# Optimization experiments

Measured on AMD Instinct MI355X. Metric: run time of the kernel, lower is better.

The kernel has to match this reference:

```python
import jax, jax.numpy as jnp
import numpy as np

H, HD, CHUNK = 16, 64, 128


def _rotary(x):
    # x: (B,H,N,d); rotary_embedding_torch default: interleaved pairs, theta=10000
    N, d = x.shape[-2], x.shape[-1]
    inv_freq = 1.0 / (10000.0 ** (jnp.arange(0, d, 2, dtype=jnp.float32) / d))
    ang = jnp.arange(N, dtype=jnp.float32)[:, None] * inv_freq[None, :]  # (N, d/2)
    ang = jnp.repeat(ang, 2, axis=-1)  # (N, d), each freq repeated twice
    cos, sin = jnp.cos(ang), jnp.sin(ang)
    x1, x2 = x[..., 0::2], x[..., 1::2]
    xr = jnp.stack([-x2, x1], axis=-1).reshape(x.shape)  # rotate_half (interleaved)
    return x * cos + xr * sin


def _split_heads(t, B, N):
    return t.reshape(B, N, H, HD).transpose(0, 2, 1, 3)  # (B,H,N,Hd)


def _chunked(Q, KK, VK):
    # chunk-parallel linear-attention recurrence: per-token outer products,
    # intra-chunk cumsum, carried state across chunks, Frobenius normalization.
    B, h, N, d = Q.shape
    nc = N // CHUNK

    def to_chunks(t):
        return t.reshape(B, h, nc, CHUNK, d).transpose(2, 0, 1, 3, 4)  # (nc,B,h,c,d)

    S0 = jnp.eye(d, dtype=Q.dtype) * jnp.sqrt(jnp.float32(d))
    S0 = jnp.broadcast_to(S0, (B, h, d, d))

    def step(SK_state, inp):
        q, kk, vk = inp  # (B,h,c,d)
        ok = jnp.einsum('bhni,bhnj->bhnij', kk, vk)            # outer products
        SK = jnp.cumsum(ok, axis=2) + SK_state[:, :, None]      # prefix-sum + carry
        norm = jnp.sqrt(jnp.sum(SK * SK, axis=(-2, -1), keepdims=True)) + 1e-8
        SKn = SK / norm                                         # Frobenius-normalized
        y = jnp.einsum('bhni,bhnji->bhnj', q, SKn)              # q @ SK^T per token
        return SK[:, :, -1], y

    _, ys = jax.lax.scan(step, S0, (to_chunks(Q), to_chunks(KK), to_chunks(VK)))
    return ys.transpose(1, 2, 0, 3, 4).reshape(B, h, N, d)


def setup_inputs():
    key = jax.random.key(0)
    ks = jax.random.split(key, 5)
    B, N, D = 2, 2048, 1024
    X = jax.random.normal(ks[0], (B, N, D), jnp.float32)
    w_qkv = jax.random.normal(ks[1], (D, 3 * H * HD), jnp.float32) * 0.02
    w_kvkv = jax.random.normal(ks[2], (D, 4 * H * HD), jnp.float32) * 0.02
    w_out = jax.random.normal(ks[3], (H * HD, D), jnp.float32) * 0.02
    b_out = jnp.zeros((D,), jnp.float32)
    return {"X": X, "w_qkv": w_qkv, "w_kvkv": w_kvkv, "w_out": w_out, "b_out": b_out}


def reference(X, w_qkv, w_kvkv, w_out, b_out):
    B, N, D = X.shape
    q, k, v = jnp.split(X @ w_qkv, 3, axis=-1)
    Q = _split_heads(q, B, N)
    K = _split_heads(k, B, N)
    V = _split_heads(v, B, N)
    kk, vk, _kv, _vv = jnp.split(X @ w_kvkv, 4, axis=-1)
    KK = _split_heads(kk, B, N)
    VK = _split_heads(vk, B, N)
    # NOTE: the SV branch (KV, VV) in the original is returned by the chunked fn
    # but never used by forward's output, so it is dead code for the fwd result.
    Qn = _chunked(Q, KK, VK)
    Qr = _rotary(Qn)
    Kr = _rotary(K)
    scale = 1.0 / jnp.sqrt(jnp.float32(HD))
    scores = jnp.einsum('bhqd,bhkd->bhqk', Qr, Kr) * scale
    mask = jnp.tril(jnp.ones((N, N), dtype=bool))
    scores = jnp.where(mask, scores, -jnp.inf)
    attn = jax.nn.softmax(scores, axis=-1)
    out = jnp.einsum('bhqk,bhkd->bhqd', attn, V)
    out = out.transpose(0, 2, 1, 3).reshape(B, N, H * HD)
    return out @ w_out + b_out
```

## Files before the change

### kernel.cpp

```cpp
#include <hip/hip_runtime.h>

typedef unsigned int u32;
typedef unsigned short u16;
typedef __attribute__((ext_vector_type(8))) __bf16 bf16x8;
typedef __attribute__((ext_vector_type(4))) float f32x4;

constexpr int NH = 16;
constexpr int HDM = 64;
constexpr int NSQ = 2048;
constexpr int KD = 1024;
constexpr int BHT = 32;
constexpr float ROT_C = 13.287712379549449f / 32.0f;

__device__ __forceinline__ u16 f2bf(float f) {
  u32 u = __float_as_uint(f);
  u += 0x7fffu + ((u >> 16) & 1u);
  return (u16)(u >> 16);
}
__device__ __forceinline__ float bf2f(u16 h) {
  return __uint_as_float(((u32)h) << 16);
}

__device__ __forceinline__ void fast_sincos(float th, float* s, float* c) {
  __sincosf(th, s, c);
}

__device__ __forceinline__ void gl_lds16(const u16* g, u16* l) {
  __builtin_amdgcn_global_load_lds(
      (const __attribute__((address_space(1))) u32*)g,
      (__attribute__((address_space(3))) u32*)l, 16, 0, 0);
}

__device__ __forceinline__ bf16x8 ldf(const u16* b, int row, int cb, int rs) {
  return *(const bf16x8*)((const char*)b + row * rs + ((cb * 16) ^ ((row & 7) << 4)));
}

__global__ void k_f32_to_bf16(const float* __restrict__ src, u16* __restrict__ dst, int n4) {
  int i = blockIdx.x * 256 + threadIdx.x;
  if (i < n4) {
    float4 v = ((const float4*)src)[i];
    ushort4 o;
    o.x = f2bf(v.x); o.y = f2bf(v.y); o.z = f2bf(v.z); o.w = f2bf(v.w);
    ((ushort4*)dst)[i] = o;
  }
}

__global__ void k_transpose_bf16(const float* __restrict__ src, int srcld,
                                 u16* __restrict__ dst, int dstld) {
  __shared__ float tile[64][65];
  int ct = blockIdx.x * 64, kt = blockIdx.y * 64;
  int lc = threadIdx.x & 63, rg = threadIdx.x >> 6;
#pragma unroll
  for (int i = 0; i < 16; ++i) {
    int kl = rg * 16 + i;
    tile[kl][lc] = src[(size_t)(kt + kl) * srcld + ct + lc];
  }
  __syncthreads();
#pragma unroll
  for (int i = 0; i < 16; ++i) {
    int cl = rg * 16 + i;
    dst[(size_t)(ct + cl) * dstld + kt + lc] = f2bf(tile[lc][cl]);
  }
}

__device__ __forceinline__ void stage256(const u16* __restrict__ gA, const u16* __restrict__ gB,
                                         u16* AL, u16* BL, int mt, int nt, int kt, int tid) {
#pragma unroll
  for (int l = 0; l < 4; ++l) {
    int off = l * 8192 + tid * 16;
    int row = off >> 7;
    int cb = (off >> 4) & 7;
    int col = (cb ^ (row & 7)) << 3;
    gl_lds16(gA + (size_t)(mt * 256 + row) * KD + kt * 64 + col, AL + (off >> 1));
  }
#pragma unroll
  for (int l = 0; l < 4; ++l) {
    int off = l * 8192 + tid * 16;
    int row = off >> 7;
    int cb = (off >> 4) & 7;
    int col = (cb ^ (row & 7)) << 3;
    gl_lds16(gB + (size_t)(nt * 256 + row) * KD + kt * 64 + col, BL + (off >> 1));
  }
}

__device__ __forceinline__ void compute256(const u16* AL, const u16* BL,
                                           f32x4 (&acc)[8][4], int wr, int wc, int g, int q) {
#pragma unroll
  for (int ks = 0; ks < 2; ++ks) {
    bf16x8 bfr[4];
#pragma unroll
    for (int nf = 0; nf < 4; ++nf)
      bfr[nf] = ldf(BL, wc * 64 + nf * 16 + q, ks * 4 + g, 128);
#pragma unroll
    for (int mh = 0; mh < 2; ++mh) {
      bf16x8 af[4];
#pragma unroll
      for (int mf = 0; mf < 4; ++mf)
        af[mf] = ldf(AL, wr * 128 + (mh * 4 + mf) * 16 + q, ks * 4 + g, 128);
      __builtin_amdgcn_s_setprio(1);
#pragma unroll
      for (int mf = 0; mf < 4; ++mf)
#pragma unroll
        for (int nf = 0; nf < 4; ++nf)
          acc[mh * 4 + mf][nf] =
              __builtin_amdgcn_mfma_f32_16x16x32_bf16(af[mf], bfr[nf], acc[mh * 4 + mf][nf], 0, 0, 0);
      __builtin_amdgcn_s_setprio(0);
    }
  }
}

__global__ __launch_bounds__(512) void k_gemm0_256(const u16* __restrict__ A,
                                                   const u16* __restrict__ Bt,
                                                   u16* __restrict__ o0, u16* __restrict__ o1,
                                                   u16* __restrict__ o2, u16* __restrict__ o3,
                                                   u16* __restrict__ o4) {
  __shared__ __align__(16) u16 AL[2][16384];
  __shared__ __align__(16) u16 BL[2][16384];
  int bid = blockIdx.x;
  int swz = (bid & 7) * 40 + (bid >> 3);
  int nt = swz % 20, mt = swz / 20;
  int tid = threadIdx.x, w = tid >> 6, lane = tid & 63;
  int g = lane >> 4, q = lane & 15;
  int wr = w >> 2, wc = w & 3;

  f32x4 acc[8][4];
#pragma unroll
  for (int m = 0; m < 8; ++m)
#pragma unroll
    for (int n = 0; n < 4; ++n) acc[m][n] = (f32x4){0.f, 0.f, 0.f, 0.f};

  stage256(A, Bt, AL[0], BL[0], mt, nt, 0, tid);
  stage256(A, Bt, AL[1], BL[1], mt, nt, 1, tid);
  asm volatile("s_waitcnt vmcnt(8)" ::: "memory");
  __builtin_amdgcn_s_barrier();
  __builtin_amdgcn_sched_barrier(0);

#define GBODY(KT, PBUF)                                                     \
  {                                                                         \
    compute256(AL[PBUF], BL[PBUF], acc, wr, wc, g, q);                      \
    __builtin_amdgcn_s_barrier();                                           \
    if ((KT) + 2 < 16) {                                                    \
      stage256(A, Bt, AL[PBUF], BL[PBUF], mt, nt, (KT) + 2, tid);           \
      asm volatile("s_waitcnt vmcnt(8)" ::: "memory");                      \
    } else if ((KT) == 14) {                                                \
      asm volatile("s_waitcnt vmcnt(0)" ::: "memory");                      \
    }                                                                       \
    __builtin_amdgcn_s_barrier();                                           \
    __builtin_amdgcn_sched_barrier(0);                                      \
  }

  for (int it = 0; it < 8; ++it) {
    GBODY(2 * it, 0);
    GBODY(2 * it + 1, 1);
  }
#undef GBODY

#pragma unroll
  for (int nf = 0; nf < 4; ++nf) {
    int c = nt * 256 + wc * 64 + nf * 16 + q;
    int t = c >> 10;
    if (t == 1) {
      int rem = c & 1023;
      int hh = rem >> 6, dd = rem & 63;
      float invf = exp2f(-(float)(dd >> 1) * ROT_C);
      float sgn = (dd & 1) ? 1.0f : -1.0f;
      size_t hoff = (size_t)hh * NSQ * HDM + dd;
#pragma unroll
      for (int mf = 0; mf < 8; ++mf)
#pragma unroll
        for (int r = 0; r < 4; ++r) {
          int row = mt * 256 + wr * 128 + mf * 16 + g * 4 + r;
          int b = row >> 11, nn = row & 2047;
          float mine = acc[mf][nf][r];
          float part = __shfl_xor(mine, 1);
          float s, cc;
          fast_sincos((float)nn * invf, &s, &cc);
          o1[(size_t)b * NH * NSQ * HDM + hoff + (size_t)nn * HDM] = f2bf(mine * cc + sgn * part * s);
        }
    } else if (t == 2) {
      int rem = c & 1023;
      int hh = rem >> 6, dd = rem & 63;
#pragma unroll
      for (int mf = 0; mf < 8; ++mf)
#pragma unroll
        for (int r = 0; r < 4; ++r) {
          int row = mt * 256 + wr * 128 + mf * 16 + g * 4 + r;
          int b = row >> 11, nn = row & 2047;
          o2[((size_t)(b * NH + hh) * HDM + dd) * NSQ + nn] = f2bf(acc[mf][nf][r]);
        }
    } else {
      u16* dst = (t == 0) ? o0 : ((t == 3) ? o3 : o4);
      int rem = c & 1023;
      size_t hoff = (size_t)(rem >> 6) * NSQ * HDM + (rem & 63);
#pragma unroll
      for (int mf = 0; mf < 8; ++mf)
#pragma unroll
        for (int r = 0; r < 4; ++r) {
          int row = mt * 256 + wr * 128 + mf * 16 + g * 4 + r;
          int b = row >> 11, nn = row & 2047;
          dst[(size_t)b * NH * NSQ * HDM + hoff + (size_t)nn * HDM] = f2bf(acc[mf][nf][r]);
        }
    }
  }
}

__device__ __forceinline__ void gemm_stage1(const u16* __restrict__ A, const u16* __restrict__ Bt,
                                            u16* Albuf, u16* Blbuf, int mt, int nt, int kt,
                                            int w, int lane) {
#pragma unroll
  for (int i = 0; i < 2; ++i) {
    int ob = (w * 2 + i) * 1024 + lane * 16;
    int row = ob >> 6;
    int ke = (ob & 63) >> 1;
    int grow = mt * 128 + row;
    int k = kt * 32 + ke;
    const u16* ga = A + ((size_t)((grow >> 11) * NH + (k >> 6)) * NSQ + (grow & 2047)) * HDM + (k & 63);
    gl_lds16(ga, Albuf + (w * 2 + i) * 512);
    const u16* gb = Bt + (size_t)(nt * 128 + row) * KD + kt * 32 + ke;
    gl_lds16(gb, Blbuf + (w * 2 + i) * 512);
  }
}

__device__ __forceinline__ void gemm_compute1(const u16* Albuf, const u16* Blbuf,
                                              f32x4 acc[4][4], int wr, int wc, int g, int q) {
  bf16x8 af[4], bfr[4];
#pragma unroll
  for (int m = 0; m < 4; ++m)
    af[m] = *(const bf16x8*)(Albuf + (wr * 64 + m * 16 + q) * 32 + g * 8);
#pragma unroll
  for (int n = 0; n < 4; ++n)
    bfr[n] = *(const bf16x8*)(Blbuf + (wc * 64 + n * 16 + q) * 32 + g * 8);
#pragma unroll
  for (int m = 0; m < 4; ++m)
#pragma unroll
    for (int n = 0; n < 4; ++n)
      acc[m][n] = __builtin_amdgcn_mfma_f32_16x16x32_bf16(af[m], bfr[n], acc[m][n], 0, 0, 0);
}

__global__ __launch_bounds__(256) void k_gemm_out(const u16* __restrict__ A, const u16* __restrict__ Bt,
                                                  const float* __restrict__ bias,
                                                  float* __restrict__ Cout) {
  __shared__ __align__(16) u16 Al[2][4096];
  __shared__ __align__(16) u16 Bl[2][4096];
  int nt = blockIdx.x, mt = blockIdx.y;
  int tid = threadIdx.x, w = tid >> 6, lane = tid & 63;
  int g = lane >> 4, q = lane & 15, wr = w >> 1, wc = w & 1;
  f32x4 acc[4][4];
#pragma unroll
  for (int m = 0; m < 4; ++m)
#pragma unroll
    for (int n = 0; n < 4; ++n) acc[m][n] = (f32x4){0.f, 0.f, 0.f, 0.f};

  gemm_stage1(A, Bt, Al[0], Bl[0], mt, nt, 0, w, lane);
  __syncthreads();
  int cur = 0;
  for (int kt = 1; kt < 32; ++kt) {
    gemm_stage1(A, Bt, Al[cur ^ 1], Bl[cur ^ 1], mt, nt, kt, w, lane);
    gemm_compute1(Al[cur], Bl[cur], acc, wr, wc, g, q);
    __syncthreads();
    cur ^= 1;
  }
  gemm_compute1(Al[cur], Bl[cur], acc, wr, wc, g, q);

#pragma unroll
  for (int nf = 0; nf < 4; ++nf) {
    int c = nt * 128 + wc * 64 + nf * 16 + q;
    float bv = bias[c];
#pragma unroll
    for (int mf = 0; mf < 4; ++mf)
#pragma unroll
      for (int r = 0; r < 4; ++r) {
        int row = mt * 128 + wr * 64 + mf * 16 + g * 4 + r;
        Cout[(size_t)row * 1024 + c] = acc[mf][nf][r] + bv;
      }
  }
}

__global__ __launch_bounds__(256) void k_chunk_outer(const u16* __restrict__ Kk,
                                                     const u16* __restrict__ Vk,
                                                     float* __restrict__ Mc) {
  int bhc = blockIdx.x;
  __shared__ float kk[128][64];
  __shared__ float vv[128][64];
  int tid = threadIdx.x;
  size_t base = ((size_t)(bhc >> 4) * NSQ + (size_t)(bhc & 15) * 128) * HDM;
  for (int i = tid; i < 2048; i += 256) {
    int r = i >> 4, c4 = (i & 15) * 4;
    ushort4 a = ((const ushort4*)(Kk + base))[i];
    kk[r][c4] = bf2f(a.x); kk[r][c4 + 1] = bf2f(a.y); kk[r][c4 + 2] = bf2f(a.z); kk[r][c4 + 3] = bf2f(a.w);
    ushort4 b = ((const ushort4*)(Vk + base))[i];
    vv[r][c4] = bf2f(b.x); vv[r][c4 + 1] = bf2f(b.y); vv[r][c4 + 2] = bf2f(b.z); vv[r][c4 + 3] = bf2f(b.w);
  }
  __syncthreads();
  int i0 = (tid >> 4) * 4, j0 = (tid & 15) * 4;
  float a2[4][4];
#pragma unroll
  for (int di = 0; di < 4; ++di)
#pragma unroll
    for (int dj = 0; dj < 4; ++dj) a2[di][dj] = 0.f;
  for (int m = 0; m < 128; ++m) {
    float ka[4], vb[4];
#pragma unroll
    for (int d = 0; d < 4; ++d) { ka[d] = kk[m][i0 + d]; vb[d] = vv[m][j0 + d]; }
#pragma unroll
    for (int di = 0; di < 4; ++di)
#pragma unroll
      for (int dj = 0; dj < 4; ++dj) a2[di][dj] += ka[di] * vb[dj];
  }
  float* out = Mc + (size_t)bhc * 4096;
#pragma unroll
  for (int di = 0; di < 4; ++di) {
    float4 v = make_float4(a2[di][0], a2[di][1], a2[di][2], a2[di][3]);
    *(float4*)(out + (i0 + di) * 64 + j0) = v;
  }
}

__global__ __launch_bounds__(256) void k_chunk_prefix2(const float* __restrict__ Mc,
                                                       float* __restrict__ Sst) {
  int bh = blockIdx.x, rg = blockIdx.y;
  int tid = threadIdx.x;
  int r8 = tid >> 5, cp = tid & 31;
  int i = rg * 8 + r8, j0 = cp * 2;
  float s0 = (i == j0) ? 8.0f : 0.0f;
  float s1 = (i == j0 + 1) ? 8.0f : 0.0f;
  size_t rowoff = (size_t)i * 64 + j0;
  for (int c = 0; c < 16; ++c) {
    size_t o = ((size_t)bh * 16 + c) * 4096 + rowoff;
    *(float2*)(Sst + o) = make_float2(s0, s1);
    float2 mv = *(const float2*)(Mc + o);
    s0 += mv.x; s1 += mv.y;
  }
}

__global__ __launch_bounds__(256) void k_chunk_norm(const u16* __restrict__ Kk,
                                                    const u16* __restrict__ Vk,
                                                    const float* __restrict__ Sst,
                                                    float* __restrict__ Invn) {
  __shared__ __align__(16) u16 KkL[128 * 64];
  __shared__ __align__(16) u16 VkL[128 * 64];
  __shared__ __align__(16) u16 SL[64 * 64];
  __shared__ float prebuf[128][2];
  __shared__ float bilbuf[128][2];
  __shared__ float sc[128];
  __shared__ float red[4];
  int bhc = blockIdx.x;
  int tid = threadIdx.x, w = tid >> 6, lane = tid & 63;
  int g = lane >> 4, q = lane & 15;
  size_t base = (size_t)bhc * 8192;

  for (int ic = tid; ic < 1024; ic += 256) {
    int row = ic >> 3, cb = ic & 7;
    int off = row * 128 + ((cb * 16) ^ ((row & 7) << 4));
    *(uint4*)((char*)KkL + off) = ((const uint4*)(Kk + base))[ic];
    *(uint4*)((char*)VkL + off) = ((const uint4*)(Vk + base))[ic];
  }
  float ss = 0.f;
  const float4* Sg = (const float4*)(Sst + (size_t)bhc * 4096);
  for (int i = tid; i < 1024; i += 256) {
    float4 v = Sg[i];
    ss += v.x * v.x + v.y * v.y + v.z * v.z + v.w * v.w;
    int row = i >> 4, c8 = (i & 15) * 8;
    u32 lo = (u32)f2bf(v.x) | ((u32)f2bf(v.y) << 16);
    u32 hi = (u32)f2bf(v.z) | ((u32)f2bf(v.w) << 16);
    *(uint2*)((char*)SL + row * 128 + (c8 ^ ((row & 7) << 4))) = make_uint2(lo, hi);
  }
#pragma unroll
  for (int d = 1; d < 64; d <<= 1) ss += __shfl_xor(ss, d);
  if (lane == 0) red[w] = ss;
  __syncthreads();

  int wr = w >> 1, wc = w & 1;
  bf16x8 ka[4][2], va[4][2];
#pragma unroll
  for (int mf = 0; mf < 4; ++mf)
#pragma unroll
    for (int ks = 0; ks < 2; ++ks) {
      ka[mf][ks] = ldf(KkL, wr * 64 + mf * 16 + q, ks * 4 + g, 128);
      va[mf][ks] = ldf(VkL, wr * 64 + mf * 16 + q, ks * 4 + g, 128);
    }

  float pracc[4][4];
#pragma unroll
  for (int mf = 0; mf < 4; ++mf)
#pragma unroll
    for (int r = 0; r < 4; ++r) pracc[mf][r] = 0.f;
  for (int pf = 0; pf < 4; ++pf) {
    bf16x8 kb0 = ldf(KkL, wc * 64 + pf * 16 + q, g, 128);
    bf16x8 kb1 = ldf(KkL, wc * 64 + pf * 16 + q, 4 + g, 128);
    bf16x8 vb0 = ldf(VkL, wc * 64 + pf * 16 + q, g, 128);
    bf16x8 vb1 = ldf(VkL, wc * 64 + pf * 16 + q, 4 + g, 128);
#pragma unroll
    for (int mf = 0; mf < 4; ++mf) {
      f32x4 a1 = (f32x4){0.f, 0.f, 0.f, 0.f}, b1 = (f32x4){0.f, 0.f, 0.f, 0.f};
      a1 = __builtin_amdgcn_mfma_f32_16x16x32_bf16(ka[mf][0], kb0, a1, 0, 0, 0);
      a1 = __builtin_amdgcn_mfma_f32_16x16x32_bf16(ka[mf][1], kb1, a1, 0, 0, 0);
      b1 = __builtin_amdgcn_mfma_f32_16x16x32_bf16(va[mf][0], vb0, b1, 0, 0, 0);
      b1 = __builtin_amdgcn_mfma_f32_16x16x32_bf16(va[mf][1], vb1, b1, 0, 0, 0);
#pragma unroll
      for (int r = 0; r < 4; ++r) {
        int m = wr * 64 + mf * 16 + g * 4 + r;
        int p = wc * 64 + pf * 16 + q;
        float gv = a1[r] * b1[r];
        float coef = (p < m) ? 1.f : ((p == m) ? 0.5f : 0.f);
        pracc[mf][r] += coef * gv;
      }
    }
  }
#pragma unroll
  for (int mf = 0; mf < 4; ++mf)
#pragma unroll
    for (int r = 0; r < 4; ++r) {
      float v = pracc[mf][r];
      v += __shfl_xor(v, 1); v += __shfl_xor(v, 2); v += __shfl_xor(v, 4); v += __shfl_xor(v, 8);
      pracc[mf][r] = v;
    }
  if (q == 0) {
#pragma unroll
    for (int mf = 0; mf < 4; ++mf)
#pragma unroll
      for (int r = 0; r < 4; ++r) prebuf[wr * 64 + mf * 16 + g * 4 + r][wc] = pracc[mf][r];
  }

  float bacc[4][4];
#pragma unroll
  for (int mf = 0; mf < 4; ++mf)
#pragma unroll
    for (int r = 0; r < 4; ++r) bacc[mf][r] = 0.f;
  for (int jf = 0; jf < 2; ++jf) {
    bf16x8 sb0 = ldf(SL, wc * 32 + jf * 16 + q, g, 128);
    bf16x8 sb1 = ldf(SL, wc * 32 + jf * 16 + q, 4 + g, 128);
#pragma unroll
    for (int mf = 0; mf < 4; ++mf) {
      f32x4 u = (f32x4){0.f, 0.f, 0.f, 0.f};
      u = __builtin_amdgcn_mfma_f32_16x16x32_bf16(va[mf][0], sb0, u, 0, 0, 0);
      u = __builtin_amdgcn_mfma_f32_16x16x32_bf16(va[mf][1], sb1, u, 0, 0, 0);
#pragma unroll
      for (int r = 0; r < 4; ++r) {
        int m = wr * 64 + mf * 16 + g * 4 + r;
        int j = wc * 32 + jf * 16 + q;
        float kkv = bf2f(*(const u16*)((const char*)KkL + m * 128 + ((j * 2) ^ ((m & 7) << 4))));
        bacc[mf][r] += u[r] * kkv;
      }
    }
  }
#pragma unroll
  for (int mf = 0; mf < 4; ++mf)
#pragma unroll
    for (int r = 0; r < 4; ++r) {
      float v = bacc[mf][r];
      v += __shfl_xor(v, 1); v += __shfl_xor(v, 2); v += __shfl_xor(v, 4); v += __shfl_xor(v, 8);
      bacc[mf][r] = v;
    }
  if (q == 0) {
#pragma unroll
    for (int mf = 0; mf < 4; ++mf)
#pragma unroll
      for (int r = 0; r < 4; ++r) bilbuf[wr * 64 + mf * 16 + g * 4 + r][wc] = bacc[mf][r];
  }
  __syncthreads();

  if (tid < 128)
    sc[tid] = 2.f * (prebuf[tid][0] + prebuf[tid][1] + bilbuf[tid][0] + bilbuf[tid][1]);
  __syncthreads();
  for (int off = 1; off < 128; off <<= 1) {
    float add = 0.f;
    if (tid < 128 && tid >= off) add = sc[tid - off];
    __syncthreads();
    if (tid < 128) sc[tid] += add;
    __syncthreads();
  }
  if (tid < 128) {
    float n0 = red[0] + red[1] + red[2] + red[3];
    float cum = n0 + sc[tid];
    Invn[(size_t)bhc * 128 + tid] = 1.f / (sqrtf(cum) + 1e-8f);
  }
}

__global__ __launch_bounds__(256) void k_chunk_yv2(const u16* __restrict__ Qb,
                                                   const u16* __restrict__ Kk,
                                                   const u16* __restrict__ Vk,
                                                   const float* __restrict__ Sst,
                                                   const float* __restrict__ Invn,
                                                   u16* __restrict__ Qro) {
  __shared__ __align__(16) u16 QL[128 * 64];
  __shared__ __align__(16) u16 WL[128 * 64];
  __shared__ __align__(16) u16 SL[64 * 64];
  __shared__ __align__(16) u16 PL[128 * 128];
  __shared__ float inv[128];
  int bhc = blockIdx.x;
  int tid = threadIdx.x, w = tid >> 6, lane = tid & 63;
  int g = lane >> 4, q = lane & 15;
  size_t base = (size_t)bhc * 8192;

  for (int ic = tid; ic < 1024; ic += 256) {
    int row = ic >> 3, cb = ic & 7;
    int off = row * 128 + ((cb * 16) ^ ((row & 7) << 4));
    *(uint4*)((char*)QL + off) = ((const uint4*)(Qb + base))[ic];
    *(uint4*)((char*)WL + off) = ((const uint4*)(Vk + base))[ic];
  }
  const float4* Sg = (const float4*)(Sst + (size_t)bhc * 4096);
  for (int i = tid; i < 1024; i += 256) {
    float4 v = Sg[i];
    int row = i >> 4, c8 = (i & 15) * 8;
    u32 lo = (u32)f2bf(v.x) | ((u32)f2bf(v.y) << 16);
    u32 hi = (u32)f2bf(v.z) | ((u32)f2bf(v.w) << 16);
    *(uint2*)((char*)SL + row * 128 + (c8 ^ ((row & 7) << 4))) = make_uint2(lo, hi);
  }
  if (tid < 128) inv[tid] = Invn[(size_t)bhc * 128 + tid];
  __syncthreads();

  int wr = w >> 1, wc = w & 1;
  f32x4 pacc[4][4];
#pragma unroll
  for (int mf = 0; mf < 4; ++mf)
#pragma unroll
    for (int nf = 0; nf < 4; ++nf) pacc[mf][nf] = (f32x4){0.f, 0.f, 0.f, 0.f};
#pragma unroll
  for (int ks = 0; ks < 2; ++ks) {
    bf16x8 av[4], bq[4];
#pragma unroll
    for (int mf = 0; mf < 4; ++mf) av[mf] = ldf(WL, wr * 64 + mf * 16 + q, ks * 4 + g, 128);
#pragma unroll
    for (int nf = 0; nf < 4; ++nf) bq[nf] = ldf(QL, wc * 64 + nf * 16 + q, ks * 4 + g, 128);
#pragma unroll
    for (int mf = 0; mf < 4; ++mf)
#pragma unroll
      for (int nf = 0; nf < 4; ++nf)
        pacc[mf][nf] = __builtin_amdgcn_mfma_f32_16x16x32_bf16(av[mf], bq[nf], pacc[mf][nf], 0, 0, 0);
  }
#pragma unroll
  for (int mf = 0; mf < 4; ++mf)
#pragma unroll
    for (int nf = 0; nf < 4; ++nf) {
      int m0 = wr * 64 + mf * 16 + g * 4;
      int n = wc * 64 + nf * 16 + q;
      float v0 = (m0 + 0 <= n) ? pacc[mf][nf][0] : 0.f;
      float v1 = (m0 + 1 <= n) ? pacc[mf][nf][1] : 0.f;
      float v2 = (m0 + 2 <= n) ? pacc[mf][nf][2] : 0.f;
      float v3 = (m0 + 3 <= n) ? pacc[mf][nf][3] : 0.f;
      u32 lo = (u32)f2bf(v0) | ((u32)f2bf(v1) << 16);
      u32 hi = (u32)f2bf(v2) | ((u32)f2bf(v3) << 16);
      *(uint2*)((char*)PL + n * 256 + ((m0 * 2) ^ ((n & 7) << 4))) = make_uint2(lo, hi);
    }
  __syncthreads();
  for (int i = tid; i < 2048; i += 256) {
    int r = i >> 4, c4 = (i & 15) * 4;
    ushort4 kv = ((const ushort4*)(Kk + base))[i];
    *(u16*)((char*)WL + (c4 + 0) * 256 + ((r * 2) ^ (((c4 + 0) & 7) << 4))) = kv.x;
    *(u16*)((char*)WL + (c4 + 1) * 256 + ((r * 2) ^ (((c4 + 1) & 7) << 4))) = kv.y;
    *(u16*)((char*)WL + (c4 + 2) * 256 + ((r * 2) ^ (((c4 + 2) & 7) << 4))) = kv.z;
    *(u16*)((char*)WL + (c4 + 3) * 256 + ((r * 2) ^ (((c4 + 3) & 7) << 4))) = kv.w;
  }
  __syncthreads();

  f32x4 yacc[4][2];
#pragma unroll
  for (int nf = 0; nf < 4; ++nf)
#pragma unroll
    for (int jf = 0; jf < 2; ++jf) yacc[nf][jf] = (f32x4){0.f, 0.f, 0.f, 0.f};
#pragma unroll
  for (int ks = 0; ks < 2; ++ks) {
    bf16x8 aq[4], bs[2];
#pragma unroll
    for (int nf = 0; nf < 4; ++nf) aq[nf] = ldf(QL, wr * 64 + nf * 16 + q, ks * 4 + g, 128);
#pragma unroll
    for (int jf = 0; jf < 2; ++jf) bs[jf] = ldf(SL, wc * 32 + jf * 16 + q, ks * 4 + g, 128);
#pragma unroll
    for (int nf = 0; nf < 4; ++nf)
#pragma unroll
      for (int jf = 0; jf < 2; ++jf)
        yacc[nf][jf] = __builtin_amdgcn_mfma_f32_16x16x32_bf16(aq[nf], bs[jf], yacc[nf][jf], 0, 0, 0);
  }
#pragma unroll
  for (int ks = 0; ks < 4; ++ks) {
    bf16x8 ap[4], bk[2];
#pragma unroll
    for (int nf = 0; nf < 4; ++nf) ap[nf] = ldf(PL, wr * 64 + nf * 16 + q, ks * 4 + g, 256);
#pragma unroll
    for (int jf = 0; jf < 2; ++jf) bk[jf] = ldf(WL, wc * 32 + jf * 16 + q, ks * 4 + g, 256);
#pragma unroll
    for (int nf = 0; nf < 4; ++nf)
#pragma unroll
      for (int jf = 0; jf < 2; ++jf)
        yacc[nf][jf] = __builtin_amdgcn_mfma_f32_16x16x32_bf16(ap[nf], bk[jf], yacc[nf][jf], 0, 0, 0);
  }
#pragma unroll
  for (int nf = 0; nf < 4; ++nf)
#pragma unroll
    for (int jf = 0; jf < 2; ++jf) {
      int j = wc * 32 + jf * 16 + q;
      float invf = exp2f(-(float)(j >> 1) * ROT_C);
      float sgn = (j & 1) ? 1.0f : -1.0f;
#pragma unroll
      for (int r = 0; r < 4; ++r) {
        int n = wr * 64 + nf * 16 + g * 4 + r;
        float val = yacc[nf][jf][r] * inv[n];
        float part = __shfl_xor(val, 1);
        int ng = (bhc & 15) * 128 + n;
        float s, cc;
        fast_sincos((float)ng * invf, &s, &cc);
        Qro[base + (size_t)n * 64 + j] = f2bf((val * cc + sgn * part * s) * 0.125f);
      }
    }
}

__global__ __launch_bounds__(512) void k_attn2(const u16* __restrict__ Qr, const u16* __restrict__ Kr,
                                               const u16* __restrict__ Vt, u16* __restrict__ Ob) {
  __shared__ __align__(16) u16 QL[128 * 64];
  __shared__ __align__(16) u16 KL[2][64 * 64];
  __shared__ __align__(16) u16 VL[2][64 * 64];
  __shared__ __align__(16) u16 PLa[8][16 * 64];
  int bh = blockIdx.x, pair = blockIdx.y;
  int tid = threadIdx.x, w = tid >> 6, lane = tid & 63;
  int g = lane >> 4, q16 = lane & 15;
  const u16* Qg_base = Qr + (size_t)bh * NSQ * HDM;
  const u16* Kg_base = Kr + (size_t)bh * NSQ * HDM;
  const u16* VTg_base = Vt + (size_t)bh * HDM * NSQ;
  u16* Og_base = Ob + (size_t)bh * NSQ * HDM;
  u16* Pw = PLa[w];
  int srow = tid >> 3, scb = tid & 7;

  for (int phase = 0; phase < 2; ++phase) {
    int t = phase ? (15 - pair) : pair;
    int qbase = t * 128;
    int nkt = 2 * t + 2;
    int lastkt_w = (qbase + w * 16 + 15) >> 6;
    int qg_ = qbase + w * 16 + q16;

    {
      const u16* Qg = Qg_base + qbase * 64;
#pragma unroll
      for (int it = 0; it < 2; ++it) {
        int c = it * 512 + tid;
        int row = c >> 3, cb = c & 7;
        gl_lds16(Qg + row * 64 + ((cb ^ (row & 7)) << 3), QL + c * 8);
      }
    }
    gl_lds16(Kg_base + srow * 64 + ((scb ^ (srow & 7)) << 3), KL[0] + tid * 8);
    gl_lds16(VTg_base + (size_t)srow * NSQ + ((scb ^ (srow & 7)) << 3), VL[0] + tid * 8);
    __syncthreads();

    bf16x8 qf[2];
    qf[0] = ldf(QL, w * 16 + q16, g, 128);
    qf[1] = ldf(QL, w * 16 + q16, 4 + g, 128);

    f32x4 o[4];
#pragma unroll
    for (int df = 0; df < 4; ++df) o[df] = (f32x4){0.f, 0.f, 0.f, 0.f};
    float m_run = -3.0e38f, l_run = 0.f;

    int cur = 0;
    for (int kt = 0; kt < nkt; ++kt) {
      if (kt + 1 < nkt) {
        gl_lds16(Kg_base + (kt + 1) * 4096 + srow * 64 + ((scb ^ (srow & 7)) << 3),
                 KL[cur ^ 1] + tid * 8);
        gl_lds16(VTg_base + (size_t)srow * NSQ + (kt + 1) * 64 + ((scb ^ (srow & 7)) << 3),
                 VL[cur ^ 1] + tid * 8);
      }
      if (kt <= lastkt_w) {
        const u16* Kbuf = KL[cur];
        const u16* Vbuf = VL[cur];
        f32x4 st[4];
#pragma unroll
        for (int kf = 0; kf < 4; ++kf) {
          f32x4 s = (f32x4){0.f, 0.f, 0.f, 0.f};
          s = __builtin_amdgcn_mfma_f32_16x16x32_bf16(ldf(Kbuf, kf * 16 + q16, g, 128), qf[0], s, 0, 0, 0);
          s = __builtin_amdgcn_mfma_f32_16x16x32_bf16(ldf(Kbuf, kf * 16 + q16, 4 + g, 128), qf[1], s, 0, 0, 0);
          st[kf] = s;
        }
        float smax = -1e30f;
        bool needmask = (kt * 64 + 63 > qbase + w * 16);
        if (needmask) {
#pragma unroll
          for (int kf = 0; kf < 4; ++kf)
#pragma unroll
            for (int r = 0; r < 4; ++r) {
              int keyg = kt * 64 + kf * 16 + g * 4 + r;
              float sv = st[kf][r];
              sv = (keyg <= qg_) ? sv : -1e30f;
              st[kf][r] = sv;
              smax = fmaxf(smax, sv);
            }
        } else {
#pragma unroll
          for (int kf = 0; kf < 4; ++kf)
#pragma unroll
            for (int r = 0; r < 4; ++r) smax = fmaxf(smax, st[kf][r]);
        }
        smax = fmaxf(smax, __shfl_xor(smax, 16));
        smax = fmaxf(smax, __shfl_xor(smax, 32));
        float mnew = fmaxf(m_run, smax);
        float corr = __expf(m_run - mnew);
        float ls = 0.f;
#pragma unroll
        for (int kf = 0; kf < 4; ++kf)
#pragma unroll
          for (int r = 0; r < 4; ++r) {
            float p = __expf(st[kf][r] - mnew);
            st[kf][r] = p;
            ls += p;
          }
        ls += __shfl_xor(ls, 16);
        ls += __shfl_xor(ls, 32);
        m_run = mnew;
        l_run = l_run * corr + ls;
#pragma unroll
        for (int df = 0; df < 4; ++df) {
          o[df][0] *= corr; o[df][1] *= corr; o[df][2] *= corr; o[df][3] *= corr;
        }
#pragma unroll
        for (int kf = 0; kf < 4; ++kf) {
          u32 lo = (u32)f2bf(st[kf][0]) | ((u32)f2bf(st[kf][1]) << 16);
          u32 hi = (u32)f2bf(st[kf][2]) | ((u32)f2bf(st[kf][3]) << 16);
          int ba = q16 * 128 + ((kf * 32 + g * 8) ^ ((q16 & 7) << 4));
          *(u32*)((char*)Pw + ba) = lo;
          *(u32*)((char*)Pw + ba + 4) = hi;
        }
#pragma unroll
        for (int kc = 0; kc < 2; ++kc) {
          bf16x8 pf = ldf(Pw, q16, kc * 4 + g, 128);
#pragma unroll
          for (int df = 0; df < 4; ++df) {
            bf16x8 vf = ldf(Vbuf, df * 16 + q16, kc * 4 + g, 128);
            o[df] = __builtin_amdgcn_mfma_f32_16x16x32_bf16(vf, pf, o[df], 0, 0, 0);
          }
        }
      }
      __syncthreads();
      cur ^= 1;
    }
    float invl = 1.0f / l_run;
    u16* Og = Og_base + (size_t)(qbase + w * 16 + q16) * HDM;
#pragma unroll
    for (int df = 0; df < 4; ++df)
#pragma unroll
      for (int r = 0; r < 4; ++r) Og[df * 16 + g * 4 + r] = f2bf(o[df][r] * invl);
  }
}

extern "C" void kernel_launch(void* const* d_in, const int* in_sizes, int n_in,
                              void* d_out, int out_size, void* d_ws, size_t ws_size,
                              hipStream_t stream) {
  const float* X = (const float*)d_in[0];
  const float* w_qkv = (const float*)d_in[1];
  const float* w_kvkv = (const float*)d_in[2];
  const float* w_out = (const float*)d_in[3];
  const float* b_out = (const float*)d_in[4];
  float* out = (float*)d_out;
  char* ws = (char*)d_ws;

  u16* Xb  = (u16*)(ws + 0);
  u16* WbT = (u16*)(ws + 8388608);
  u16* WoT = (u16*)(ws + 18874368);
  u16* Qb  = (u16*)(ws + 20971520);
  float* Sst = (float*)(ws + 29360128);
  u16* Vtb = (u16*)(ws + 37748736);
  u16* Kkb = (u16*)(ws + 46137344);
  u16* Vkb = (u16*)(ws + 54525952);
  u16* Kr  = (u16*)(ws + 62914560);
  u16* Qr  = (u16*)(ws + 71303168);
  float* Mc   = (float*)(ws + 8388608);
  float* Invn = (float*)(ws + 16777216);
  u16* Ob = (u16*)(ws + 0);
  (void)in_sizes; (void)n_in; (void)out_size; (void)ws_size;

  k_f32_to_bf16<<<dim3(4096), dim3(256), 0, stream>>>(X, Xb, 1048576);
  k_transpose_bf16<<<dim3(48, 16), dim3(256), 0, stream>>>(w_qkv, 3072, WbT, 1024);
  k_transpose_bf16<<<dim3(32, 16), dim3(256), 0, stream>>>(w_kvkv, 4096, WbT + (size_t)3072 * 1024, 1024);
  k_transpose_bf16<<<dim3(16, 16), dim3(256), 0, stream>>>(w_out, 1024, WoT, 1024);
  k_gemm0_256<<<dim3(320), dim3(512), 0, stream>>>(Xb, WbT, Qb, Kr, Vtb, Kkb, Vkb);
  k_chunk_outer<<<dim3(512), dim3(256), 0, stream>>>(Kkb, Vkb, Mc);
  k_chunk_prefix2<<<dim3(32, 8), dim3(256), 0, stream>>>(Mc, Sst);
  k_chunk_norm<<<dim3(512), dim3(256), 0, stream>>>(Kkb, Vkb, Sst, Invn);
  k_chunk_yv2<<<dim3(512), dim3(256), 0, stream>>>(Qb, Kkb, Vkb, Sst, Invn, Qr);
  k_attn2<<<dim3(32, 8), dim3(512), 0, stream>>>(Qr, Kr, Vtb, Ob);
  k_gemm_out<<<dim3(8, 32), dim3(256), 0, stream>>>(Ob, WoT, b_out, out);
}
```

Baseline: 196.8 us.

## Split GEMM0 K-tile into half-chunk LDS stages with finer-grained prefetch interleave

Restructures the fused QKV projection GEMM so each 64-wide K tile is stored as two 32-wide halves with a new swizzle, and global-to-LDS loads for the next halves are issued between the four MFMA sub-phases. The intent is to spread memory traffic evenly across compute and overlap loads with MFMA work more tightly, hiding load latency. It adds more barriers per K step, which may increase synchronisation overhead, and relies on the vmcnt accounting staying correct.

New measurement: 207.9 us. +5.6%, slower.

```diff
diff --git a/kernel.cpp b/kernel.cpp
--- a/kernel.cpp
+++ b/kernel.cpp
@@ -33,6 +33,10 @@
 
 __device__ __forceinline__ bf16x8 ldf(const u16* b, int row, int cb, int rs) {
   return *(const bf16x8*)((const char*)b + row * rs + ((cb * 16) ^ ((row & 7) << 4)));
+}
+
+__device__ __forceinline__ bf16x8 ldh(const u16* Lbase, int row, int g) {
+  return *(const bf16x8*)((const char*)Lbase + row * 64 + ((g ^ ((row >> 1) & 3)) << 4));
 }
 
 __global__ void k_f32_to_bf16(const float* __restrict__ src, u16* __restrict__ dst, int n4) {
@@ -63,49 +67,14 @@
   }
 }
 
-__device__ __forceinline__ void stage256(const u16* __restrict__ gA, const u16* __restrict__ gB,
-                                         u16* AL, u16* BL, int mt, int nt, int kt, int tid) {
-#pragma unroll
-  for (int l = 0; l < 4; ++l) {
-    int off = l * 8192 + tid * 16;
-    int row = off >> 7;
-    int cb = (off >> 4) & 7;
-    int col = (cb ^ (row & 7)) << 3;
-    gl_lds16(gA + (size_t)(mt * 256 + row) * KD + kt * 64 + col, AL + (off >> 1));
-  }
-#pragma unroll
-  for (int l = 0; l < 4; ++l) {
-    int off = l * 8192 + tid * 16;
-    int row = off >> 7;
-    int cb = (off >> 4) & 7;
-    int col = (cb ^ (row & 7)) << 3;
-    gl_lds16(gB + (size_t)(nt * 256 + row) * KD + kt * 64 + col, BL + (off >> 1));
-  }
-}
-
-__device__ __forceinline__ void compute256(const u16* AL, const u16* BL,
-                                           f32x4 (&acc)[8][4], int wr, int wc, int g, int q) {
-#pragma unroll
-  for (int ks = 0; ks < 2; ++ks) {
-    bf16x8 bfr[4];
-#pragma unroll
-    for (int nf = 0; nf < 4; ++nf)
-      bfr[nf] = ldf(BL, wc * 64 + nf * 16 + q, ks * 4 + g, 128);
-#pragma unroll
-    for (int mh = 0; mh < 2; ++mh) {
-      bf16x8 af[4];
-#pragma unroll
-      for (int mf = 0; mf < 4; ++mf)
-        af[mf] = ldf(AL, wr * 128 + (mh * 4 + mf) * 16 + q, ks * 4 + g, 128);
-      __builtin_amdgcn_s_setprio(1);
-#pragma unroll
-      for (int mf = 0; mf < 4; ++mf)
-#pragma unroll
-        for (int nf = 0; nf < 4; ++nf)
-          acc[mh * 4 + mf][nf] =
-              __builtin_amdgcn_mfma_f32_16x16x32_bf16(af[mf], bfr[nf], acc[mh * 4 + mf][nf], 0, 0, 0);
-      __builtin_amdgcn_s_setprio(0);
-    }
+__device__ __forceinline__ void stage_half(const u16* __restrict__ g, int tbase,
+                                           u16* Ldst, int kt, int ch, int tid) {
+#pragma unroll
+  for (int l = 0; l < 2; ++l) {
+    int i = tid + l * 512;
+    int row = i >> 2, cp = i & 3;
+    int c = cp ^ ((row >> 1) & 3);
+    gl_lds16(g + (size_t)(tbase + row) * KD + kt * 64 + ch * 32 + c * 8, Ldst + i * 8);
   }
 }
 
@@ -114,14 +83,15 @@
                                                    u16* __restrict__ o0, u16* __restrict__ o1,
                                                    u16* __restrict__ o2, u16* __restrict__ o3,
                                                    u16* __restrict__ o4) {
-  __shared__ __align__(16) u16 AL[2][16384];
-  __shared__ __align__(16) u16 BL[2][16384];
+  __shared__ __align__(16) u16 AL[2][2][8192];
+  __shared__ __align__(16) u16 BL[2][2][8192];
   int bid = blockIdx.x;
   int swz = (bid & 7) * 40 + (bid >> 3);
   int nt = swz % 20, mt = swz / 20;
   int tid = threadIdx.x, w = tid >> 6, lane = tid & 63;
   int g = lane >> 4, q = lane & 15;
   int wr = w >> 2, wc = w & 3;
+  int mb = mt * 256, nb = nt * 256;
 
   f32x4 acc[8][4];
 #pragma unroll
@@ -129,31 +99,85 @@
 #pragma unroll
     for (int n = 0; n < 4; ++n) acc[m][n] = (f32x4){0.f, 0.f, 0.f, 0.f};
 
-  stage256(A, Bt, AL[0], BL[0], mt, nt, 0, tid);
-  stage256(A, Bt, AL[1], BL[1], mt, nt, 1, tid);
-  asm volatile("s_waitcnt vmcnt(8)" ::: "memory");
-  __builtin_amdgcn_s_barrier();
+  stage_half(A, mb, AL[0][0], 0, 0, tid);
+  stage_half(Bt, nb, BL[0][0], 0, 0, tid);
+  stage_half(A, mb, AL[0][1], 0, 1, tid);
+  stage_half(Bt, nb, BL[0][1], 0, 1, tid);
+  stage_half(A, mb, AL[1][0], 1, 0, tid);
+  stage_half(Bt, nb, BL[1][0], 1, 0, tid);
+  asm volatile("s_waitcnt vmcnt(4)" ::: "memory");
+  asm volatile("s_barrier" ::: "memory");
   __builtin_amdgcn_sched_barrier(0);
 
-#define GBODY(KT, PBUF)                                                     \
-  {                                                                         \
-    compute256(AL[PBUF], BL[PBUF], acc, wr, wc, g, q);                      \
-    __builtin_amdgcn_s_barrier();                                           \
-    if ((KT) + 2 < 16) {                                                    \
-      stage256(A, Bt, AL[PBUF], BL[PBUF], mt, nt, (KT) + 2, tid);           \
-      asm volatile("s_waitcnt vmcnt(8)" ::: "memory");                      \
-    } else if ((KT) == 14) {                                                \
-      asm volatile("s_waitcnt vmcnt(0)" ::: "memory");                      \
-    }                                                                       \
-    __builtin_amdgcn_s_barrier();                                           \
-    __builtin_amdgcn_sched_barrier(0);                                      \
-  }
-
-  for (int it = 0; it < 8; ++it) {
-    GBODY(2 * it, 0);
-    GBODY(2 * it + 1, 1);
-  }
-#undef GBODY
+  for (int kt = 0; kt < 16; ++kt) {
+    int db = kt & 1;
+    bf16x8 bfr[4], af[4];
+
+#pragma unroll
+    for (int nf = 0; nf < 4; ++nf) bfr[nf] = ldh(BL[db][0], wc * 64 + nf * 16 + q, g);
+#pragma unroll
+    for (int mf = 0; mf < 4; ++mf) af[mf] = ldh(AL[db][0], wr * 128 + mf * 16 + q, g);
+    if (kt < 15) stage_half(A, mb, AL[db ^ 1][1], kt + 1, 1, tid);
+    asm volatile("s_barrier" ::: "memory");
+    __builtin_amdgcn_sched_barrier(0);
+    __builtin_amdgcn_s_setprio(1);
+#pragma unroll
+    for (int mf = 0; mf < 4; ++mf)
+#pragma unroll
+      for (int nf = 0; nf < 4; ++nf)
+        acc[mf][nf] = __builtin_amdgcn_mfma_f32_16x16x32_bf16(af[mf], bfr[nf], acc[mf][nf], 0, 0, 0);
+    __builtin_amdgcn_s_setprio(0);
+    asm volatile("s_barrier" ::: "memory");
+
+#pragma unroll
+    for (int mf = 0; mf < 4; ++mf) af[mf] = ldh(AL[db][0], wr * 128 + (4 + mf) * 16 + q, g);
+    if (kt < 15) stage_half(Bt, nb, BL[db ^ 1][1], kt + 1, 1, tid);
+    asm volatile("s_barrier" ::: "memory");
+    __builtin_amdgcn_sched_barrier(0);
+    __builtin_amdgcn_s_setprio(1);
+#pragma unroll
+    for (int mf = 0; mf < 4; ++mf)
+#pragma unroll
+      for (int nf = 0; nf < 4; ++nf)
+        acc[4 + mf][nf] = __builtin_amdgcn_mfma_f32_16x16x32_bf16(af[mf], bfr[nf], acc[4 + mf][nf], 0, 0, 0);
+    __builtin_amdgcn_s_setprio(0);
+    asm volatile("s_barrier" ::: "memory");
+
+#pragma unroll
+    for (int nf = 0; nf < 4; ++nf) bfr[nf] = ldh(BL[db][1], wc * 64 + nf * 16 + q, g);
+#pragma unroll
+    for (int mf = 0; mf < 4; ++mf) af[mf] = ldh(AL[db][1], wr * 128 + mf * 16 + q, g);
+    if (kt < 14) stage_half(A, mb, AL[db][0], kt + 2, 0, tid);
+    asm volatile("s_barrier" ::: "memory");
+    __builtin_amdgcn_sched_barrier(0);
+    __builtin_amdgcn_s_setprio(1);
+#pragma unroll
+    for (int mf = 0; mf < 4; ++mf)
+#pragma unroll
+      for (int nf = 0; nf < 4; ++nf)
+        acc[mf][nf] = __builtin_amdgcn_mfma_f32_16x16x32_bf16(af[mf], bfr[nf], acc[mf][nf], 0, 0, 0);
+    __builtin_amdgcn_s_setprio(0);
+    asm volatile("s_barrier" ::: "memory");
+
+#pragma unroll
+    for (int mf = 0; mf < 4; ++mf) af[mf] = ldh(AL[db][1], wr * 128 + (4 + mf) * 16 + q, g);
+    if (kt < 14) {
+      stage_half(Bt, nb, BL[db][0], kt + 2, 0, tid);
+      asm volatile("s_waitcnt vmcnt(4)" ::: "memory");
+    } else if (kt == 14) {
+      asm volatile("s_waitcnt vmcnt(0)" ::: "memory");
+    }
+    asm volatile("s_barrier" ::: "memory");
+    __builtin_amdgcn_sched_barrier(0);
+    __builtin_amdgcn_s_setprio(1);
+#pragma unroll
+    for (int mf = 0; mf < 4; ++mf)
+#pragma unroll
+      for (int nf = 0; nf < 4; ++nf)
+        acc[4 + mf][nf] = __builtin_amdgcn_mfma_f32_16x16x32_bf16(af[mf], bfr[nf], acc[4 + mf][nf], 0, 0, 0);
+    __builtin_amdgcn_s_setprio(0);
+    asm volatile("s_barrier" ::: "memory");
+  }
 
 #pragma unroll
   for (int nf = 0; nf < 4; ++nf) {
```
